# Performance work log

Measured on AMD Instinct MI355X. Metric: run time of the kernel, lower is better.

Reference implementation:

```python
import jax, jax.numpy as jnp
import numpy as np

E = 40000   # num_entities
R = 474     # num_relations
D = 200     # Config.embedding_dim
L = 100     # n_num_lit
B = 32      # batch

def setup_inputs() -> dict:
    key = jax.random.key(0)
    ks = jax.random.split(key, 11)
    return {
        "e1": jax.random.randint(ks[0], (B, 1), 0, E),
        "rel": jax.random.randint(ks[1], (B, 1), 0, R),
        "emb_e": jax.random.normal(ks[2], (E, D), jnp.float32) * 0.1,           # emb_e.weight
        "emb_rel": jax.random.normal(ks[3], (R, D), jnp.float32) * 0.1,         # emb_rel.weight
        "num_lit": jax.random.normal(ks[4], (E, L), jnp.float32),               # numerical_literals (raw)
        "num_lit_norm": jax.random.uniform(ks[5], (E, L), jnp.float32),         # numerical_literals_normalized
        "W_lit": jax.random.normal(ks[6], (D, D + L), jnp.float32) / np.float32(np.sqrt(D + L)),  # emb_num_lit.weight
        "b_lit": jnp.zeros((D,), jnp.float32),                                  # emb_num_lit.bias
        "c": jax.random.normal(ks[7], (L,), jnp.float32),                       # RBF centers (fixed)
        "var": jax.random.uniform(ks[8], (L,), jnp.float32, minval=0.5, maxval=2.0),  # RBF variances (fixed)
        "nf_w": jax.random.normal(ks[9], (R, L), jnp.float32) * 0.1,            # nf_weights.weight
    }

def reference(e1, rel, emb_e, emb_rel, num_lit, num_lit_norm, W_lit, b_lit, c, var, nf_w):
    e1f = e1.reshape(-1)    # (B,)
    relf = rel.reshape(-1)  # (B,)
    # LiteralE gating via linear layer: emb_num_lit(cat([emb, lit]))
    e1_emb = jnp.concatenate([emb_e[e1f], num_lit_norm[e1f]], axis=1) @ W_lit.T + b_lit  # (B, D)
    e2_multi_emb = jnp.concatenate([emb_e, num_lit_norm], axis=1) @ W_lit.T + b_lit      # (E, D)
    rel_emb = emb_rel[relf]                                                              # (B, D)
    # dropout is identity at inference
    score_l = (e1_emb * rel_emb) @ e2_multi_emb.T  # (B, E)
    # KBLN numerical-literal score: broadcast diff + RBF + weighted reduction over literals
    n = num_lit[e1f][:, None, :] - num_lit[None, :, :]   # (B, E, L) -- large intermediate
    phi = jnp.exp(-jnp.square(n - c) / var)              # RBF, pointwise
    score_n = jnp.einsum('bel,bl->be', phi, nf_w[relf])  # bmm(phi, w_nf^T).squeeze()
    return jax.nn.sigmoid(score_l + score_n)             # (B, E)
```

## Files before the change

kernel.cpp:

```cpp
#include <hip/hip_runtime.h>
#include <math.h>

#define E_N 40000
#define D_N 200
#define L_N 100
#define K_N 300
#define B_N 32

typedef float  f32x4 __attribute__((ext_vector_type(4)));
typedef short  s16x8 __attribute__((ext_vector_type(8)));

#define WS_SH 0
#define WS_W  3200
#define WS_NR 6400
#define WS_S0 6500
#define WS_PA 6532

#define SM_CB  6532
#define SM_TOT 7044

__device__ inline float fast_exp2(float x) {
#if __has_builtin(__builtin_amdgcn_exp2f)
    return __builtin_amdgcn_exp2f(x);
#else
    return exp2f(x);
#endif
}
__device__ inline float fast_rcp(float x) {
#if __has_builtin(__builtin_amdgcn_rcpf)
    return __builtin_amdgcn_rcpf(x);
#else
    return 1.0f / x;
#endif
}
__device__ inline ushort f2bf(float f) {
    uint u = __builtin_bit_cast(uint, f);
    u += 0x7fffu + ((u >> 16) & 1u);
    return (ushort)(u >> 16);
}
__device__ inline s16x8 pack_bf8(f32x4 lo, f32x4 hi) {
    s16x8 bb;
    bb[0] = (short)f2bf(lo[0]); bb[1] = (short)f2bf(lo[1]);
    bb[2] = (short)f2bf(lo[2]); bb[3] = (short)f2bf(lo[3]);
    bb[4] = (short)f2bf(hi[0]); bb[5] = (short)f2bf(hi[1]);
    bb[6] = (short)f2bf(hi[2]); bb[7] = (short)f2bf(hi[3]);
    return bb;
}

__global__ __launch_bounds__(320) void prep_kernel(
    const int* __restrict__ e1, const int* __restrict__ rel,
    const float* __restrict__ emb_e, const float* __restrict__ emb_rel,
    const float* __restrict__ num_lit, const float* __restrict__ num_lit_norm,
    const float* __restrict__ W, const float* __restrict__ b_lit,
    const float* __restrict__ c, const float* __restrict__ var,
    const float* __restrict__ nf_w, float* __restrict__ ws)
{
    const int b = blockIdx.x;
    const int t = threadIdx.x;
    __shared__ float q[D_N];
    const int e1b = e1[b];
    const int rb  = rel[b];

    if (t < D_N) {
        const float* wr = W + t * K_N;
        const float* er = emb_e + (long)e1b * D_N;
        const float* nl = num_lit_norm + (long)e1b * L_N;
        float s0_ = b_lit[t], s1_ = 0.f, s2_ = 0.f, s3_ = 0.f;
        for (int k = 0; k < D_N; k += 4) {
            s0_ += er[k+0] * wr[k+0]; s1_ += er[k+1] * wr[k+1];
            s2_ += er[k+2] * wr[k+2]; s3_ += er[k+3] * wr[k+3];
        }
        for (int k = 0; k < L_N; k += 4) {
            s0_ += nl[k+0] * wr[D_N+k+0]; s1_ += nl[k+1] * wr[D_N+k+1];
            s2_ += nl[k+2] * wr[D_N+k+2]; s3_ += nl[k+3] * wr[D_N+k+3];
        }
        q[t] = ((s0_ + s1_) + (s2_ + s3_)) * emb_rel[rb * D_N + t];
    }
    __syncthreads();

    {
        float pk = 0.f;
        if (t < K_N) {
            float a0 = 0.f, a1 = 0.f, a2 = 0.f, a3 = 0.f;
            for (int d = 0; d < D_N; d += 4) {
                a0 += q[d+0] * W[(d+0) * K_N + t];
                a1 += q[d+1] * W[(d+1) * K_N + t];
                a2 += q[d+2] * W[(d+2) * K_N + t];
                a3 += q[d+3] * W[(d+3) * K_N + t];
            }
            pk = (a0 + a1) + (a2 + a3);
        }
        const int s  = t >> 5;
        const int g  = (t >> 3) & 3;
        const int j  = t & 7;
        const int mt = b >> 4;
        const int ln = (g << 4) | (b & 15);
        ushort* pa = (ushort*)(ws + WS_PA);
        pa[((mt * 10 + s) * 64 + ln) * 8 + j] = f2bf(pk);
    }

    if (t < L_N) {
        const float r = sqrtf(1.4426950408889634f / var[t]);
        ws[WS_SH + t * 32 + b] = r * (num_lit[(long)e1b * L_N + t] - c[t]);
        ws[WS_W  + t * 32 + b] = nf_w[rb * L_N + t];
        if (b == 0) ws[WS_NR + t] = -r;
    }
    if (t == 300) {
        float s = 0.f;
        for (int d = 0; d < D_N; ++d) s += q[d] * b_lit[d];
        ws[WS_S0 + b] = s;
    }
}

__global__ __launch_bounds__(256, 4) void score_kernel(
    const float* __restrict__ emb_e, const float* __restrict__ num_lit,
    const float* __restrict__ num_lit_norm, const float* __restrict__ ws,
    float* __restrict__ out)
{
    __shared__ float smem[SM_TOT];

    const int lane = threadIdx.x & 63;
    const int wv   = threadIdx.x >> 6;
    const int mt   = wv & 1;
    const int h    = wv >> 1;
    const int eg   = blockIdx.x;
    const int er   = lane & 15;
    const int g    = lane >> 4;
    const int e    = eg * 16 + er;
    const int b0   = mt * 16 + 4 * g;

    {
        const f32x4* s4 = (const f32x4*)ws;
        f32x4* d4 = (f32x4*)smem;
        for (int i = threadIdx.x; i < 1633; i += 256) d4[i] = s4[i];
    }
    __syncthreads();

    f32x4 acc = {0.f, 0.f, 0.f, 0.f};
    if (h == 0) acc = *(const f32x4*)(ws + WS_S0 + b0);

    s16x8 afr[5];
    {
        const s16x8* pAg = (const s16x8*)(ws + WS_PA);
#pragma unroll
        for (int i = 0; i < 5; ++i) afr[i] = pAg[(mt * 10 + h * 5 + i) * 64 + lane];
    }

    const float* embr = emb_e        + (long)e * D_N;
    const float* litn = num_lit_norm + (long)e * L_N;

#pragma unroll
    for (int i = 0; i < 4; ++i) {
        const int k0 = 32 * (h * 5 + i) + 8 * g;
        const float* bp = (k0 < 200) ? (embr + k0) : (litn + (k0 - 200));
        f32x4 lo = *(const f32x4*)bp;
        f32x4 hi = *(const f32x4*)(bp + 4);
        acc = __builtin_amdgcn_mfma_f32_16x16x32_bf16(afr[i], pack_bf8(lo, hi), acc, 0, 0, 0);
    }
    if (h == 0) {
        const int k0 = 128 + 8 * g;
        f32x4 lo = *(const f32x4*)(embr + k0);
        f32x4 hi = *(const f32x4*)(embr + k0 + 4);
        acc = __builtin_amdgcn_mfma_f32_16x16x32_bf16(afr[4], pack_bf8(lo, hi), acc, 0, 0, 0);
    } else {
        f32x4 z = {0.f, 0.f, 0.f, 0.f};
        f32x4 lo = z, hi = z;
        if (g == 0)      { lo = *(const f32x4*)(litn + 88); hi = *(const f32x4*)(litn + 92); }
        else if (g == 1) { lo = *(const f32x4*)(litn + 96); }
        acc = __builtin_amdgcn_mfma_f32_16x16x32_bf16(afr[4], pack_bf8(lo, hi), acc, 0, 0, 0);
    }

    const int lc0 = h ? 13 : 0;
    const int lcE = h ? 25 : 13;
    const f32x4* m4 = (const f32x4*)(num_lit + (long)e * L_N);
    f32x4 mv_a = m4[lc0];
    f32x4 mv_b = m4[lc0 + 1];
    for (int lc = lc0; lc < lcE; ++lc) {
        const f32x4 mv = mv_a;
        mv_a = mv_b;
        if (lc + 2 < lcE) mv_b = m4[lc + 2];
        const f32x4 nv = *(const f32x4*)(smem + WS_NR + lc * 4);
#pragma unroll
        for (int ll = 0; ll < 4; ++ll) {
            const int l = lc * 4 + ll;
            const float rm = nv[ll] * mv[ll];
            f32x4 s4v = *(const f32x4*)(smem + WS_SH + l * 32 + b0);
            f32x4 w4v = *(const f32x4*)(smem + WS_W  + l * 32 + b0);
#pragma unroll
            for (int j = 0; j < 4; ++j) {
                const float u = rm + s4v[j];
                acc[j] = fmaf(fast_exp2(-(u * u)), w4v[j], acc[j]);
            }
        }
    }

    float* cbuf = smem + SM_CB;
    if (h) {
        *(f32x4*)(cbuf + (mt * 64 + lane) * 4) = acc;
    }
    __syncthreads();
    if (!h) {
        const f32x4 o = *(const f32x4*)(cbuf + (mt * 64 + lane) * 4);
#pragma unroll
        for (int j = 0; j < 4; ++j) {
            const float v = acc[j] + o[j];
            const float z = fast_exp2(v * -1.4426950408889634f);
            out[(long)(b0 + j) * E_N + e] = fast_rcp(1.0f + z);
        }
    }
}

extern "C" void kernel_launch(void* const* d_in, const int* in_sizes, int n_in,
                              void* d_out, int out_size, void* d_ws, size_t ws_size,
                              hipStream_t stream) {
    const int*   e1       = (const int*)d_in[0];
    const int*   rel      = (const int*)d_in[1];
    const float* emb_e    = (const float*)d_in[2];
    const float* emb_rel  = (const float*)d_in[3];
    const float* num_lit  = (const float*)d_in[4];
    const float* num_lit_norm = (const float*)d_in[5];
    const float* W_lit    = (const float*)d_in[6];
    const float* b_lit    = (const float*)d_in[7];
    const float* c        = (const float*)d_in[8];
    const float* var      = (const float*)d_in[9];
    const float* nf_w     = (const float*)d_in[10];
    float* out = (float*)d_out;
    float* ws  = (float*)d_ws;

    hipLaunchKernelGGL(prep_kernel, dim3(B_N), dim3(320), 0, stream,
                       e1, rel, emb_e, emb_rel, num_lit, num_lit_norm,
                       W_lit, b_lit, c, var, nf_w, ws);
    hipLaunchKernelGGL(score_kernel, dim3(2500), dim3(256), 0, stream,
                       emb_e, num_lit, num_lit_norm, ws, out);
}
```

Before: 46.58 us.

## Process two entity tiles per score block to reuse staged shared data

Each score block now handles 32 entities as two 16-entity sub-tiles with separate accumulators, halving the grid to 1250 blocks. The per-block shared-memory staging, A-fragment loads and LDS reads of shift/weight vectors are amortized over twice the work, and two independent exp/FMA chains give more ILP. It raises register use (launch bounds lowered to 3 waves/EU) and reduces block count, which may lower occupancy and load balance across CUs.

```diff
diff --git a/kernel.cpp b/kernel.cpp
--- a/kernel.cpp
+++ b/kernel.cpp
@@ -17,7 +17,7 @@
 #define WS_PA 6532
 
 #define SM_CB  6532
-#define SM_TOT 7044
+#define SM_TOT 7556
 
 __device__ inline float fast_exp2(float x) {
 #if __has_builtin(__builtin_amdgcn_exp2f)
@@ -112,7 +112,7 @@
     }
 }
 
-__global__ __launch_bounds__(256, 4) void score_kernel(
+__global__ __launch_bounds__(256, 3) void score_kernel(
     const float* __restrict__ emb_e, const float* __restrict__ num_lit,
     const float* __restrict__ num_lit_norm, const float* __restrict__ ws,
     float* __restrict__ out)
@@ -123,10 +123,10 @@
     const int wv   = threadIdx.x >> 6;
     const int mt   = wv & 1;
     const int h    = wv >> 1;
-    const int eg   = blockIdx.x;
     const int er   = lane & 15;
     const int g    = lane >> 4;
-    const int e    = eg * 16 + er;
+    const int ea   = blockIdx.x * 32 + er;
+    const int eb   = ea + 16;
     const int b0   = mt * 16 + 4 * g;
 
     {
@@ -136,8 +136,12 @@
     }
     __syncthreads();
 
-    f32x4 acc = {0.f, 0.f, 0.f, 0.f};
-    if (h == 0) acc = *(const f32x4*)(ws + WS_S0 + b0);
+    f32x4 acc_a = {0.f, 0.f, 0.f, 0.f};
+    f32x4 acc_b = {0.f, 0.f, 0.f, 0.f};
+    if (h == 0) {
+        acc_a = *(const f32x4*)(ws + WS_S0 + b0);
+        acc_b = acc_a;
+    }
 
     s16x8 afr[5];
     {
@@ -146,66 +150,87 @@
         for (int i = 0; i < 5; ++i) afr[i] = pAg[(mt * 10 + h * 5 + i) * 64 + lane];
     }
 
-    const float* embr = emb_e        + (long)e * D_N;
-    const float* litn = num_lit_norm + (long)e * L_N;
+    const float* embrA = emb_e        + (long)ea * D_N;
+    const float* litnA = num_lit_norm + (long)ea * L_N;
+    const float* embrB = emb_e        + (long)eb * D_N;
+    const float* litnB = num_lit_norm + (long)eb * L_N;
 
 #pragma unroll
     for (int i = 0; i < 4; ++i) {
         const int k0 = 32 * (h * 5 + i) + 8 * g;
-        const float* bp = (k0 < 200) ? (embr + k0) : (litn + (k0 - 200));
-        f32x4 lo = *(const f32x4*)bp;
-        f32x4 hi = *(const f32x4*)(bp + 4);
-        acc = __builtin_amdgcn_mfma_f32_16x16x32_bf16(afr[i], pack_bf8(lo, hi), acc, 0, 0, 0);
+        const float* bpA = (k0 < 200) ? (embrA + k0) : (litnA + (k0 - 200));
+        const float* bpB = (k0 < 200) ? (embrB + k0) : (litnB + (k0 - 200));
+        f32x4 loA = *(const f32x4*)bpA;
+        f32x4 hiA = *(const f32x4*)(bpA + 4);
+        f32x4 loB = *(const f32x4*)bpB;
+        f32x4 hiB = *(const f32x4*)(bpB + 4);
+        acc_a = __builtin_amdgcn_mfma_f32_16x16x32_bf16(afr[i], pack_bf8(loA, hiA), acc_a, 0, 0, 0);
+        acc_b = __builtin_amdgcn_mfma_f32_16x16x32_bf16(afr[i], pack_bf8(loB, hiB), acc_b, 0, 0, 0);
     }
     if (h == 0) {
         const int k0 = 128 + 8 * g;
-        f32x4 lo = *(const f32x4*)(embr + k0);
-        f32x4 hi = *(const f32x4*)(embr + k0 + 4);
-        acc = __builtin_amdgcn_mfma_f32_16x16x32_bf16(afr[4], pack_bf8(lo, hi), acc, 0, 0, 0);
+        f32x4 loA = *(const f32x4*)(embrA + k0);
+        f32x4 hiA = *(const f32x4*)(embrA + k0 + 4);
+        f32x4 loB = *(const f32x4*)(embrB + k0);
+        f32x4 hiB = *(const f32x4*)(embrB + k0 + 4);
+        acc_a = __builtin_amdgcn_mfma_f32_16x16x32_bf16(afr[4], pack_bf8(loA, hiA), acc_a, 0, 0, 0);
+        acc_b = __builtin_amdgcn_mfma_f32_16x16x32_bf16(afr[4], pack_bf8(loB, hiB), acc_b, 0, 0, 0);
     } else {
         f32x4 z = {0.f, 0.f, 0.f, 0.f};
-        f32x4 lo = z, hi = z;
-        if (g == 0)      { lo = *(const f32x4*)(litn + 88); hi = *(const f32x4*)(litn + 92); }
-        else if (g == 1) { lo = *(const f32x4*)(litn + 96); }
-        acc = __builtin_amdgcn_mfma_f32_16x16x32_bf16(afr[4], pack_bf8(lo, hi), acc, 0, 0, 0);
+        f32x4 loA = z, hiA = z, loB = z, hiB = z;
+        if (g == 0)      { loA = *(const f32x4*)(litnA + 88); hiA = *(const f32x4*)(litnA + 92);
+                           loB = *(const f32x4*)(litnB + 88); hiB = *(const f32x4*)(litnB + 92); }
+        else if (g == 1) { loA = *(const f32x4*)(litnA + 96);
+                           loB = *(const f32x4*)(litnB + 96); }
+        acc_a = __builtin_amdgcn_mfma_f32_16x16x32_bf16(afr[4], pack_bf8(loA, hiA), acc_a, 0, 0, 0);
+        acc_b = __builtin_amdgcn_mfma_f32_16x16x32_bf16(afr[4], pack_bf8(loB, hiB), acc_b, 0, 0, 0);
     }
 
     const int lc0 = h ? 13 : 0;
     const int lcE = h ? 25 : 13;
-    const f32x4* m4 = (const f32x4*)(num_lit + (long)e * L_N);
-    f32x4 mv_a = m4[lc0];
-    f32x4 mv_b = m4[lc0 + 1];
+    const f32x4* m4a = (const f32x4*)(num_lit + (long)ea * L_N);
+    const f32x4* m4b = (const f32x4*)(num_lit + (long)eb * L_N);
+    f32x4 pa0 = m4a[lc0], pa1 = m4a[lc0 + 1];
+    f32x4 pb0 = m4b[lc0], pb1 = m4b[lc0 + 1];
     for (int lc = lc0; lc < lcE; ++lc) {
-        const f32x4 mv = mv_a;
-        mv_a = mv_b;
-        if (lc + 2 < lcE) mv_b = m4[lc + 2];
+        const f32x4 mva = pa0; pa0 = pa1;
+        const f32x4 mvb = pb0; pb0 = pb1;
+        if (lc + 2 < lcE) { pa1 = m4a[lc + 2]; pb1 = m4b[lc + 2]; }
         const f32x4 nv = *(const f32x4*)(smem + WS_NR + lc * 4);
 #pragma unroll
         for (int ll = 0; ll < 4; ++ll) {
             const int l = lc * 4 + ll;
-            const float rm = nv[ll] * mv[ll];
+            const float rma = nv[ll] * mva[ll];
+            const float rmb = nv[ll] * mvb[ll];
             f32x4 s4v = *(const f32x4*)(smem + WS_SH + l * 32 + b0);
             f32x4 w4v = *(const f32x4*)(smem + WS_W  + l * 32 + b0);
 #pragma unroll
             for (int j = 0; j < 4; ++j) {
-                const float u = rm + s4v[j];
-                acc[j] = fmaf(fast_exp2(-(u * u)), w4v[j], acc[j]);
+                const float ua = rma + s4v[j];
+                const float ub = rmb + s4v[j];
+                acc_a[j] = fmaf(fast_exp2(-(ua * ua)), w4v[j], acc_a[j]);
+                acc_b[j] = fmaf(fast_exp2(-(ub * ub)), w4v[j], acc_b[j]);
             }
         }
     }
 
     float* cbuf = smem + SM_CB;
     if (h) {
-        *(f32x4*)(cbuf + (mt * 64 + lane) * 4) = acc;
+        *(f32x4*)(cbuf + ((0 * 2 + mt) * 64 + lane) * 4) = acc_a;
+        *(f32x4*)(cbuf + ((1 * 2 + mt) * 64 + lane) * 4) = acc_b;
     }
     __syncthreads();
     if (!h) {
-        const f32x4 o = *(const f32x4*)(cbuf + (mt * 64 + lane) * 4);
+        const f32x4 oa = *(const f32x4*)(cbuf + ((0 * 2 + mt) * 64 + lane) * 4);
+        const f32x4 ob = *(const f32x4*)(cbuf + ((1 * 2 + mt) * 64 + lane) * 4);
 #pragma unroll
         for (int j = 0; j < 4; ++j) {
-            const float v = acc[j] + o[j];
-            const float z = fast_exp2(v * -1.4426950408889634f);
-            out[(long)(b0 + j) * E_N + e] = fast_rcp(1.0f + z);
+            const float va = acc_a[j] + oa[j];
+            const float za = fast_exp2(va * -1.4426950408889634f);
+            out[(long)(b0 + j) * E_N + ea] = fast_rcp(1.0f + za);
+            const float vb = acc_b[j] + ob[j];
+            const float zb = fast_exp2(vb * -1.4426950408889634f);
+            out[(long)(b0 + j) * E_N + eb] = fast_rcp(1.0f + zb);
         }
     }
 }
@@ -230,6 +255,6 @@
     hipLaunchKernelGGL(prep_kernel, dim3(B_N), dim3(320), 0, stream,
                        e1, rel, emb_e, emb_rel, num_lit, num_lit_norm,
                        W_lit, b_lit, c, var, nf_w, ws);
-    hipLaunchKernelGGL(score_kernel, dim3(2500), dim3(256), 0, stream,
+    hipLaunchKernelGGL(score_kernel, dim3(1250), dim3(256), 0, stream,
                        emb_e, num_lit, num_lit_norm, ws, out);
 }
```

Result: no change. 46.00 us (-1.2%).

## Process four entity tiles per block and stage num_lit rows in LDS

Applied to the files above, without the earlier changes.

Each score block now handles 64 entities instead of 16, so the shared-memory preload of the per-batch tables and the A fragments is amortized over four MFMA tiles. The num_lit rows for the block are copied into LDS, and each shift/weight load from LDS is reused across four entities in the RBF loop, raising instruction-level parallelism. The cost is more registers and LDS per block, a lower launch-bounds occupancy hint, and only 625 blocks, which may underfill the GPU.

```diff
diff --git a/kernel.cpp b/kernel.cpp
--- a/kernel.cpp
+++ b/kernel.cpp
@@ -16,8 +16,8 @@
 #define WS_S0 6500
 #define WS_PA 6532
 
-#define SM_CB  6532
-#define SM_TOT 7044
+#define SM_ML  6532
+#define SM_TOT 12932
 
 __device__ inline float fast_exp2(float x) {
 #if __has_builtin(__builtin_amdgcn_exp2f)
@@ -112,7 +112,7 @@
     }
 }
 
-__global__ __launch_bounds__(256, 4) void score_kernel(
+__global__ __launch_bounds__(256, 2) void score_kernel(
     const float* __restrict__ emb_e, const float* __restrict__ num_lit,
     const float* __restrict__ num_lit_norm, const float* __restrict__ ws,
     float* __restrict__ out)
@@ -123,21 +123,27 @@
     const int wv   = threadIdx.x >> 6;
     const int mt   = wv & 1;
     const int h    = wv >> 1;
-    const int eg   = blockIdx.x;
     const int er   = lane & 15;
     const int g    = lane >> 4;
-    const int e    = eg * 16 + er;
+    const int e0   = blockIdx.x * 64 + er;
     const int b0   = mt * 16 + 4 * g;
 
     {
         const f32x4* s4 = (const f32x4*)ws;
         f32x4* d4 = (f32x4*)smem;
         for (int i = threadIdx.x; i < 1633; i += 256) d4[i] = s4[i];
-    }
-    __syncthreads();
-
-    f32x4 acc = {0.f, 0.f, 0.f, 0.f};
-    if (h == 0) acc = *(const f32x4*)(ws + WS_S0 + b0);
+        const f32x4* ml4 = (const f32x4*)(num_lit + (long)blockIdx.x * 64 * L_N);
+        for (int i = threadIdx.x; i < 1600; i += 256) d4[1633 + i] = ml4[i];
+    }
+    __syncthreads();
+
+    f32x4 acc[4];
+    {
+        f32x4 a0 = {0.f, 0.f, 0.f, 0.f};
+        if (h == 0) a0 = *(const f32x4*)(ws + WS_S0 + b0);
+#pragma unroll
+        for (int t = 0; t < 4; ++t) acc[t] = a0;
+    }
 
     s16x8 afr[5];
     {
@@ -146,66 +152,82 @@
         for (int i = 0; i < 5; ++i) afr[i] = pAg[(mt * 10 + h * 5 + i) * 64 + lane];
     }
 
-    const float* embr = emb_e        + (long)e * D_N;
-    const float* litn = num_lit_norm + (long)e * L_N;
-
-#pragma unroll
-    for (int i = 0; i < 4; ++i) {
-        const int k0 = 32 * (h * 5 + i) + 8 * g;
-        const float* bp = (k0 < 200) ? (embr + k0) : (litn + (k0 - 200));
-        f32x4 lo = *(const f32x4*)bp;
-        f32x4 hi = *(const f32x4*)(bp + 4);
-        acc = __builtin_amdgcn_mfma_f32_16x16x32_bf16(afr[i], pack_bf8(lo, hi), acc, 0, 0, 0);
-    }
-    if (h == 0) {
-        const int k0 = 128 + 8 * g;
-        f32x4 lo = *(const f32x4*)(embr + k0);
-        f32x4 hi = *(const f32x4*)(embr + k0 + 4);
-        acc = __builtin_amdgcn_mfma_f32_16x16x32_bf16(afr[4], pack_bf8(lo, hi), acc, 0, 0, 0);
-    } else {
-        f32x4 z = {0.f, 0.f, 0.f, 0.f};
-        f32x4 lo = z, hi = z;
-        if (g == 0)      { lo = *(const f32x4*)(litn + 88); hi = *(const f32x4*)(litn + 92); }
-        else if (g == 1) { lo = *(const f32x4*)(litn + 96); }
-        acc = __builtin_amdgcn_mfma_f32_16x16x32_bf16(afr[4], pack_bf8(lo, hi), acc, 0, 0, 0);
+#pragma unroll
+    for (int t = 0; t < 4; ++t) {
+        const float* embr = emb_e        + (long)(e0 + 16 * t) * D_N;
+        const float* litn = num_lit_norm + (long)(e0 + 16 * t) * L_N;
+#pragma unroll
+        for (int i = 0; i < 4; ++i) {
+            const int k0 = 32 * (h * 5 + i) + 8 * g;
+            const float* bp = (k0 < 200) ? (embr + k0) : (litn + (k0 - 200));
+            f32x4 lo = *(const f32x4*)bp;
+            f32x4 hi = *(const f32x4*)(bp + 4);
+            acc[t] = __builtin_amdgcn_mfma_f32_16x16x32_bf16(afr[i], pack_bf8(lo, hi), acc[t], 0, 0, 0);
+        }
+        if (h == 0) {
+            const int k0 = 128 + 8 * g;
+            f32x4 lo = *(const f32x4*)(embr + k0);
+            f32x4 hi = *(const f32x4*)(embr + k0 + 4);
+            acc[t] = __builtin_amdgcn_mfma_f32_16x16x32_bf16(afr[4], pack_bf8(lo, hi), acc[t], 0, 0, 0);
+        } else {
+            f32x4 z = {0.f, 0.f, 0.f, 0.f};
+            f32x4 lo = z, hi = z;
+            if (g == 0)      { lo = *(const f32x4*)(litn + 88); hi = *(const f32x4*)(litn + 92); }
+            else if (g == 1) { lo = *(const f32x4*)(litn + 96); }
+            acc[t] = __builtin_amdgcn_mfma_f32_16x16x32_bf16(afr[4], pack_bf8(lo, hi), acc[t], 0, 0, 0);
+        }
     }
 
     const int lc0 = h ? 13 : 0;
     const int lcE = h ? 25 : 13;
-    const f32x4* m4 = (const f32x4*)(num_lit + (long)e * L_N);
-    f32x4 mv_a = m4[lc0];
-    f32x4 mv_b = m4[lc0 + 1];
+    const float* ml = smem + SM_ML + er * L_N;
     for (int lc = lc0; lc < lcE; ++lc) {
-        const f32x4 mv = mv_a;
-        mv_a = mv_b;
-        if (lc + 2 < lcE) mv_b = m4[lc + 2];
-        const f32x4 nv = *(const f32x4*)(smem + WS_NR + lc * 4);
+        const f32x4 mv0 = *(const f32x4*)(ml + 0 * 16 * L_N + lc * 4);
+        const f32x4 mv1 = *(const f32x4*)(ml + 1 * 16 * L_N + lc * 4);
+        const f32x4 mv2 = *(const f32x4*)(ml + 2 * 16 * L_N + lc * 4);
+        const f32x4 mv3 = *(const f32x4*)(ml + 3 * 16 * L_N + lc * 4);
+        const f32x4 nv  = *(const f32x4*)(smem + WS_NR + lc * 4);
 #pragma unroll
         for (int ll = 0; ll < 4; ++ll) {
             const int l = lc * 4 + ll;
-            const float rm = nv[ll] * mv[ll];
+            const float rm0 = nv[ll] * mv0[ll];
+            const float rm1 = nv[ll] * mv1[ll];
+            const float rm2 = nv[ll] * mv2[ll];
+            const float rm3 = nv[ll] * mv3[ll];
             f32x4 s4v = *(const f32x4*)(smem + WS_SH + l * 32 + b0);
             f32x4 w4v = *(const f32x4*)(smem + WS_W  + l * 32 + b0);
 #pragma unroll
             for (int j = 0; j < 4; ++j) {
-                const float u = rm + s4v[j];
-                acc[j] = fmaf(fast_exp2(-(u * u)), w4v[j], acc[j]);
+                const float u0 = rm0 + s4v[j];
+                const float u1 = rm1 + s4v[j];
+                const float u2 = rm2 + s4v[j];
+                const float u3 = rm3 + s4v[j];
+                acc[0][j] = fmaf(fast_exp2(-(u0 * u0)), w4v[j], acc[0][j]);
+                acc[1][j] = fmaf(fast_exp2(-(u1 * u1)), w4v[j], acc[1][j]);
+                acc[2][j] = fmaf(fast_exp2(-(u2 * u2)), w4v[j], acc[2][j]);
+                acc[3][j] = fmaf(fast_exp2(-(u3 * u3)), w4v[j], acc[3][j]);
             }
         }
     }
 
-    float* cbuf = smem + SM_CB;
+    float* cbuf = smem + SM_ML;
+    __syncthreads();
     if (h) {
-        *(f32x4*)(cbuf + (mt * 64 + lane) * 4) = acc;
+#pragma unroll
+        for (int t = 0; t < 4; ++t)
+            *(f32x4*)(cbuf + ((t * 2 + mt) * 64 + lane) * 4) = acc[t];
     }
     __syncthreads();
     if (!h) {
-        const f32x4 o = *(const f32x4*)(cbuf + (mt * 64 + lane) * 4);
-#pragma unroll
-        for (int j = 0; j < 4; ++j) {
-            const float v = acc[j] + o[j];
-            const float z = fast_exp2(v * -1.4426950408889634f);
-            out[(long)(b0 + j) * E_N + e] = fast_rcp(1.0f + z);
+#pragma unroll
+        for (int t = 0; t < 4; ++t) {
+            const f32x4 o = *(const f32x4*)(cbuf + ((t * 2 + mt) * 64 + lane) * 4);
+#pragma unroll
+            for (int j = 0; j < 4; ++j) {
+                const float v = acc[t][j] + o[j];
+                const float z = fast_exp2(v * -1.4426950408889634f);
+                out[(long)(b0 + j) * E_N + (e0 + 16 * t)] = fast_rcp(1.0f + z);
+            }
         }
     }
 }
@@ -230,6 +252,6 @@
     hipLaunchKernelGGL(prep_kernel, dim3(B_N), dim3(320), 0, stream,
                        e1, rel, emb_e, emb_rel, num_lit, num_lit_norm,
                        W_lit, b_lit, c, var, nf_w, ws);
-    hipLaunchKernelGGL(score_kernel, dim3(2500), dim3(256), 0, stream,
+    hipLaunchKernelGGL(score_kernel, dim3(625), dim3(256), 0, stream,
                        emb_e, num_lit, num_lit_norm, ws, out);
 }
```

Result: slower. 49.88 us (+7.1%).
